# Kernel optimization log

Hardware: AMD Instinct MI355X
Metric: run time of the kernel (lower is better)

## Reference

```python
import jax, jax.numpy as jnp
import numpy as np

D_MODEL = 1024
N_HEADS = 16
D_HEAD = D_MODEL // N_HEADS
B, T = 4, 2048


def setup_inputs() -> dict:
    key = jax.random.key(0)
    ks = jax.random.split(key, 5)
    scale = 1.0 / np.sqrt(D_MODEL)
    return {
        "x": jax.random.normal(ks[0], (B, T, D_MODEL), dtype=jnp.float32),
        "W_Q": jax.random.normal(ks[1], (D_MODEL, D_MODEL), dtype=jnp.float32) * scale,
        "W_K": jax.random.normal(ks[2], (D_MODEL, D_MODEL), dtype=jnp.float32) * scale,
        "W_V": jax.random.normal(ks[3], (D_MODEL, D_MODEL), dtype=jnp.float32) * scale,
        "W_O": jax.random.normal(ks[4], (D_MODEL, D_MODEL), dtype=jnp.float32) * scale,
    }


def reference(x, W_Q, W_K, W_V, W_O):
    b, t, c = x.shape
    # nn.Linear applies x @ W.T; weights stored [out, in]
    def heads(w):
        return (x @ w.T).reshape(b, t, N_HEADS, D_HEAD).transpose(0, 2, 1, 3)  # b h t d
    q, k, v = heads(W_Q), heads(W_K), heads(W_V)
    scores = jnp.einsum("bhqd,bhkd->bhqk", q, k) / jnp.sqrt(jnp.float32(D_HEAD))
    causal = jnp.tril(jnp.ones((t, t), dtype=bool))
    scores = jnp.where(causal, scores, -jnp.inf)
    attn = jax.nn.softmax(scores, axis=-1)
    out = jnp.einsum("bhqk,bhkd->bhqd", attn, v)
    out = out.transpose(0, 2, 1, 3).reshape(b, t, c)
    return out @ W_O.T
```

## Files before the change

kernel.cpp:

```cpp
#include <hip/hip_runtime.h>
#include <stdint.h>
#include <stddef.h>

#define SEQ 2048
#define NH 16
#define DH 64
#define DM 1024
#define NROWS 8192

typedef __attribute__((ext_vector_type(4))) float f32x4;
typedef __attribute__((ext_vector_type(16))) float f32x16;
typedef __attribute__((ext_vector_type(8))) short s16x8;
typedef __attribute__((ext_vector_type(4))) unsigned u32x4;

__device__ __forceinline__ unsigned short f2bf(float f) {
  unsigned int u = __builtin_bit_cast(unsigned int, f);
  u += 0x7fffu + ((u >> 16) & 1u);
  return (unsigned short)(u >> 16);
}

__device__ __forceinline__ float exp2fast(float x) {
#if __has_builtin(__builtin_amdgcn_exp2f)
  return __builtin_amdgcn_exp2f(x);
#else
  return exp2f(x);
#endif
}

__device__ __forceinline__ float rcpfast(float x) {
#if __has_builtin(__builtin_amdgcn_rcpf)
  return __builtin_amdgcn_rcpf(x);
#else
  return 1.0f / x;
#endif
}

__device__ __forceinline__ unsigned pk2(float lo, float hi) {
  return __builtin_amdgcn_perm(__builtin_bit_cast(unsigned, hi),
                               __builtin_bit_cast(unsigned, lo), 0x07060302u);
}


__device__ __forceinline__ void async16(const void* g, void* l) {
  __builtin_amdgcn_global_load_lds(
      (const __attribute__((address_space(1))) unsigned int*)g,
      (__attribute__((address_space(3))) unsigned int*)l, 16, 0, 0);
}

__global__ __launch_bounds__(256) void cast_all(const float* __restrict__ x,
                                                const float* __restrict__ w0,
                                                const float* __restrict__ w1,
                                                const float* __restrict__ w2,
                                                const float* __restrict__ w3,
                                                short* __restrict__ Xb,
                                                short* __restrict__ Wb) {
  int g = blockIdx.x * 256 + threadIdx.x;
  const float* src;
  short* dst;
  int off;
  if (g < NROWS * DM / 8) {
    src = x; dst = Xb; off = g;
  } else {
    int r = g - NROWS * DM / 8;
    int w = r >> 17;
    off = r & 131071;
    src = (w == 0) ? w0 : (w == 1) ? w1 : (w == 2) ? w2 : w3;
    dst = Wb + ((size_t)w << 20);
  }
  const float4* s4 = (const float4*)src;
  float4 a = s4[2 * off], b = s4[2 * off + 1];
  s16x8 o;
  o[0] = (short)f2bf(a.x); o[1] = (short)f2bf(a.y);
  o[2] = (short)f2bf(a.z); o[3] = (short)f2bf(a.w);
  o[4] = (short)f2bf(b.x); o[5] = (short)f2bf(b.y);
  o[6] = (short)f2bf(b.z); o[7] = (short)f2bf(b.w);
  *(s16x8*)(dst + (size_t)8 * off) = o;
}

__global__ __launch_bounds__(512, 2) void gemm_qkv(const short* __restrict__ X,
                                                   const short* __restrict__ Wq,
                                                   const short* __restrict__ Wk,
                                                   const short* __restrict__ Wv,
                                                   short* __restrict__ Qo,
                                                   short* __restrict__ Ko,
                                                   short* __restrict__ Vo) {
  extern __shared__ __align__(16) short smem[];
  const int tid = threadIdx.x;
  const int lane = tid & 63, wave = tid >> 6;
  const int l15 = lane & 15, quad = lane >> 4;
  const int bn = blockIdx.x * 128;
  const int bm = blockIdx.y * 256;
  const int wm = (wave >> 1) * 64, wn = (wave & 1) * 64;

  const short* Ab = X + (size_t)bm * DM;
  const short* W0 = Wq + (size_t)bn * DM;
  const short* W1 = Wk + (size_t)bn * DM;
  const short* W2 = Wv + (size_t)bn * DM;

  f32x4 acc[3][4][4];
#pragma unroll
  for (int g = 0; g < 3; g++)
#pragma unroll
    for (int i = 0; i < 4; i++)
#pragma unroll
      for (int j = 0; j < 4; j++) acc[g][i][j] = (f32x4)0.f;

  auto stage = [&](int k, int buf) {
    short* base = smem + buf * 20480;
    const int k0 = k * 32;
#pragma unroll
    for (int i = 0; i < 2; i++) {
      int f = i * 512 + tid;
      int row = f >> 2;
      int c = ((f & 3) ^ (row & 3) ^ ((row >> 2) & 1)) * 8;
      async16(Ab + (size_t)row * DM + k0 + c, base + (size_t)f * 8);
    }
    {
      int f = tid;
      int row = f >> 2;
      int c = ((f & 3) ^ (row & 3) ^ ((row >> 2) & 1)) * 8;
      size_t go = (size_t)row * DM + k0 + c;
      async16(W0 + go, base + 8192 + (size_t)f * 8);
      async16(W1 + go, base + 12288 + (size_t)f * 8);
      async16(W2 + go, base + 16384 + (size_t)f * 8);
    }
  };

  stage(0, 0);
  __syncthreads();

  const int sl = (l15 & 3) ^ ((l15 >> 2) & 1);
  for (int k = 0; k < 32; k++) {
    const int buf = k & 1;
    if (k < 31) stage(k + 1, buf ^ 1);
    const short* base = smem + buf * 20480;

    s16x8 af[4];
#pragma unroll
    for (int t = 0; t < 4; t++)
      af[t] = *(const s16x8*)(base + (size_t)(wm + t * 16 + l15) * 32 + (size_t)((quad ^ sl) * 8));
#pragma unroll
    for (int g = 0; g < 3; g++) {
      const short* wb = base + 8192 + g * 4096;
      s16x8 bfr[4];
#pragma unroll
      for (int t = 0; t < 4; t++)
        bfr[t] = *(const s16x8*)(wb + (size_t)(wn + t * 16 + l15) * 32 + (size_t)((quad ^ sl) * 8));
#pragma unroll
      for (int mt = 0; mt < 4; mt++)
#pragma unroll
        for (int nt = 0; nt < 4; nt++) {
          if (g == 2)
            acc[2][mt][nt] = __builtin_amdgcn_mfma_f32_16x16x32_bf16(bfr[nt], af[mt], acc[2][mt][nt], 0, 0, 0);
          else
            acc[g][mt][nt] = __builtin_amdgcn_mfma_f32_16x16x32_bf16(af[mt], bfr[nt], acc[g][mt][nt], 0, 0, 0);
        }
    }
    __syncthreads();
  }

#pragma unroll
  for (int g = 0; g < 2; g++) {
    short* Dst = g ? Ko : Qo;
#pragma unroll
    for (int mt = 0; mt < 4; mt++)
#pragma unroll
      for (int r = 0; r < 4; r++)
#pragma unroll
        for (int nt = 0; nt < 4; nt++) {
          int m = bm + wm + mt * 16 + quad * 4 + r;
          int n = bn + wn + nt * 16 + l15;
          int b = m >> 11, t = m & (SEQ - 1);
          int hh = n >> 6, d = n & 63;
          Dst[((((size_t)b * NH + hh) * SEQ + t) << 6) + d] = (short)f2bf(acc[g][mt][nt][r]);
        }
  }
#pragma unroll
  for (int mt = 0; mt < 4; mt++)
#pragma unroll
    for (int r = 0; r < 4; r++)
#pragma unroll
      for (int nt = 0; nt < 4; nt++) {
        int n = bn + wn + nt * 16 + quad * 4 + r;
        int m = bm + wm + mt * 16 + l15;
        int b = m >> 11, t = m & (SEQ - 1);
        int hh = n >> 6, d = n & 63;
        Vo[(((size_t)b * NH + hh) * DH + d) * SEQ + t] = (short)f2bf(acc[2][mt][nt][r]);
      }
}

__global__ __launch_bounds__(256, 2) void gemm_o(const short* __restrict__ A,
                                                 const short* __restrict__ B,
                                                 float* __restrict__ C) {
  __shared__ __align__(16) short As[256 * 64];
  __shared__ __align__(16) short Bs[128 * 64];
  const int tid = threadIdx.x;
  const int lane = tid & 63, wave = tid >> 6;
  const int l15 = lane & 15, quad = lane >> 4;
  const int bm = blockIdx.y * 256, bn = blockIdx.x * 128;
  const int wm = (wave >> 1) * 128, wn = (wave & 1) * 64;

  const short* Ab = A + (size_t)bm * DM;
  const short* Bb = B + (size_t)bn * DM;

  f32x4 acc[8][4];
#pragma unroll
  for (int i = 0; i < 8; i++)
#pragma unroll
    for (int j = 0; j < 4; j++) acc[i][j] = (f32x4)0.f;

  for (int k0 = 0; k0 < DM; k0 += 64) {
#pragma unroll
    for (int i = 0; i < 8; i++) {
      int f = i * 256 + tid;
      int row = f >> 3, c = ((f & 7) ^ (row & 7)) * 8;
      async16(Ab + (size_t)row * DM + k0 + c, As + (size_t)f * 8);
    }
#pragma unroll
    for (int i = 0; i < 4; i++) {
      int f = i * 256 + tid;
      int row = f >> 3, c = ((f & 7) ^ (row & 7)) * 8;
      async16(Bb + (size_t)row * DM + k0 + c, Bs + (size_t)f * 8);
    }
    __syncthreads();
#pragma unroll
    for (int ks = 0; ks < 2; ks++) {
      s16x8 bfr[4];
#pragma unroll
      for (int t = 0; t < 4; t++)
        bfr[t] = *(const s16x8*)(Bs + (wn + t * 16 + l15) * 64 + (((ks * 4 + quad) ^ (l15 & 7)) * 8));
#pragma unroll
      for (int mt = 0; mt < 8; mt++) {
        s16x8 af = *(const s16x8*)(As + (wm + mt * 16 + l15) * 64 + (((ks * 4 + quad) ^ (l15 & 7)) * 8));
#pragma unroll
        for (int nt = 0; nt < 4; nt++)
          acc[mt][nt] = __builtin_amdgcn_mfma_f32_16x16x32_bf16(af, bfr[nt], acc[mt][nt], 0, 0, 0);
      }
    }
    __syncthreads();
  }

#pragma unroll
  for (int mt = 0; mt < 8; mt++)
#pragma unroll
    for (int r = 0; r < 4; r++) {
      int m = bm + wm + mt * 16 + quad * 4 + r;
#pragma unroll
      for (int nt = 0; nt < 4; nt++)
        C[(size_t)m * DM + bn + wn + nt * 16 + l15] = acc[mt][nt][r];
    }
}

__global__ __launch_bounds__(256, 2) void attn_kernel(const short* __restrict__ Q,
                                                      const short* __restrict__ K,
                                                      const short* __restrict__ V,
                                                      short* __restrict__ O) {
  __shared__ __align__(16) short Smem[2 * 16384];

  const int tid = threadIdx.x;
  const int lane = tid & 63, wave = tid >> 6;
  const int l31 = lane & 31, h = lane >> 5;

  const int r = blockIdx.x & 63;
  const int qt = 15 - (blockIdx.x >> 6);
  const int bh = (r & 7) * 8 + (r >> 3);
  const int q0 = qt * 128;

  const short* Qb = Q + (size_t)bh * SEQ * DH;
  const short* Kb = K + (size_t)bh * SEQ * DH;
  const short* Vb = V + (size_t)bh * DH * SEQ;

  auto stageK = [&](int ktile, int buf) {
    short* base = Smem + buf * 16384;
    const short* ksrc = Kb + (size_t)ktile * 128 * DH;
#pragma unroll
    for (int i = 0; i < 4; i++) {
      int f = i * 256 + tid;
      int kk = f >> 3, c8 = (f & 7) ^ (kk & 7);
      async16(ksrc + (size_t)kk * DH + c8 * 8, base + (size_t)f * 8);
    }
  };
  auto stageV = [&](int ktile, int buf) {
    short* base = Smem + buf * 16384 + 8192;
    const short* vsrc = Vb + (size_t)ktile * 128;
#pragma unroll
    for (int i = 0; i < 4; i++) {
      int f = i * 256 + tid;
      int d = f >> 4, c16 = (f & 15) ^ (d & 15);
      async16(vsrc + (size_t)d * SEQ + c16 * 8, base + (size_t)f * 8);
    }
  };

  s16x8 qf[4];
#pragma unroll
  for (int ks = 0; ks < 4; ks++)
    qf[ks] = *(const s16x8*)(Qb + (size_t)(q0 + wave * 32 + l31) * DH + ks * 16 + h * 8);

  f32x16 oacc[2];
  oacc[0] = (f32x16)0.f;
  oacc[1] = (f32x16)0.f;
  float m_own = -3.0e38f, l_own = 0.f, aprev = 0.f;
  s16x8 pf[8];
  const float C = 0.18033688011112042f;

  stageK(0, 0);

  for (int kt = 0; kt <= qt; kt++) {
    const int cur = kt & 1;
    __syncthreads();
    if (kt < qt) stageK(kt + 1, cur ^ 1);
    stageV(kt, cur);
    const short* Ks = Smem + cur * 16384;

    f32x16 sacc[4];
#pragma unroll
    for (int T = 0; T < 4; T++) sacc[T] = (f32x16)0.f;
#pragma unroll
    for (int ks = 0; ks < 4; ks++) {
#pragma unroll
      for (int T = 0; T < 4; T++) {
        s16x8 kf = *(const s16x8*)(Ks + (T * 32 + l31) * 64 + (((2 * ks + h) ^ (l31 & 7)) * 8));
        sacc[T] = __builtin_amdgcn_mfma_f32_32x32x16_bf16(kf, qf[ks], sacc[T], 0, 0, 0);
      }
    }

    if (kt > 0) {
      const short* Vp = Smem + (cur ^ 1) * 16384 + 8192;
#pragma unroll
      for (int r2 = 0; r2 < 16; r2++) {
        oacc[0][r2] *= aprev;
        oacc[1][r2] *= aprev;
      }
#pragma unroll
      for (int kc = 0; kc < 8; kc++) {
#pragma unroll
        for (int td = 0; td < 2; td++) {
          s16x8 vf = *(const s16x8*)(Vp + (td * 32 + l31) * 128 + (((2 * kc + h) ^ (l31 & 15)) * 8));
          oacc[td] = __builtin_amdgcn_mfma_f32_32x32x16_bf16(vf, pf[kc], oacc[td], 0, 0, 0);
        }
      }
    }

    if (kt == qt) {
      int limit = wave * 32 + l31 - 4 * h;
#pragma unroll
      for (int T = 0; T < 4; T++)
#pragma unroll
        for (int r2 = 0; r2 < 16; r2++) {
          int kkc = T * 32 + (r2 & 3) + 8 * (r2 >> 2);
          if (kkc > limit) sacc[T][r2] = -3.0e38f;
        }
    }

    float tm[4];
#pragma unroll
    for (int T = 0; T < 4; T++) {
      float a = fmaxf(fmaxf(sacc[T][0], sacc[T][1]), fmaxf(sacc[T][2], sacc[T][3]));
      float b = fmaxf(fmaxf(sacc[T][4], sacc[T][5]), fmaxf(sacc[T][6], sacc[T][7]));
      float cc = fmaxf(fmaxf(sacc[T][8], sacc[T][9]), fmaxf(sacc[T][10], sacc[T][11]));
      float d = fmaxf(fmaxf(sacc[T][12], sacc[T][13]), fmaxf(sacc[T][14], sacc[T][15]));
      tm[T] = fmaxf(fmaxf(a, b), fmaxf(cc, d));
    }
    float mx = fmaxf(fmaxf(tm[0], tm[1]), fmaxf(tm[2], tm[3]));
    mx = fmaxf(mx, __shfl_xor(mx, 32, 64));
    float mnew = fmaxf(m_own, mx);
    float mb = mnew * C;
    float alpha = exp2fast(m_own * C - mb);
    m_own = mnew;

    float ts[4];
#pragma unroll
    for (int T = 0; T < 4; T++) {
#pragma unroll
      for (int r2 = 0; r2 < 16; r2++) sacc[T][r2] = exp2fast(fmaf(sacc[T][r2], C, -mb));
      float a = (sacc[T][0] + sacc[T][1]) + (sacc[T][2] + sacc[T][3]);
      float b = (sacc[T][4] + sacc[T][5]) + (sacc[T][6] + sacc[T][7]);
      float cc = (sacc[T][8] + sacc[T][9]) + (sacc[T][10] + sacc[T][11]);
      float d = (sacc[T][12] + sacc[T][13]) + (sacc[T][14] + sacc[T][15]);
      ts[T] = (a + b) + (cc + d);
    }
    float rsum = (ts[0] + ts[1]) + (ts[2] + ts[3]);
    rsum += __shfl_xor(rsum, 32, 64);
    l_own = l_own * alpha + rsum;

#pragma unroll
    for (int T = 0; T < 4; T++) {
      unsigned P0 = pk2(sacc[T][0], sacc[T][1]);
      unsigned P1 = pk2(sacc[T][2], sacc[T][3]);
      unsigned P2 = pk2(sacc[T][4], sacc[T][5]);
      unsigned P3 = pk2(sacc[T][6], sacc[T][7]);
      unsigned P4 = pk2(sacc[T][8], sacc[T][9]);
      unsigned P5 = pk2(sacc[T][10], sacc[T][11]);
      unsigned P6 = pk2(sacc[T][12], sacc[T][13]);
      unsigned P7 = pk2(sacc[T][14], sacc[T][15]);
      unsigned R0 = (unsigned)__shfl_xor((int)(h ? P0 : P2), 32, 64);
      unsigned R1 = (unsigned)__shfl_xor((int)(h ? P1 : P3), 32, 64);
      unsigned R2 = (unsigned)__shfl_xor((int)(h ? P4 : P6), 32, 64);
      unsigned R3 = (unsigned)__shfl_xor((int)(h ? P5 : P7), 32, 64);
      u32x4 lo, hi;
      lo[0] = h ? R0 : P0; lo[1] = h ? R1 : P1; lo[2] = h ? P2 : R0; lo[3] = h ? P3 : R1;
      hi[0] = h ? R2 : P4; hi[1] = h ? R3 : P5; hi[2] = h ? P6 : R2; hi[3] = h ? P7 : R3;
      pf[2 * T] = __builtin_bit_cast(s16x8, lo);
      pf[2 * T + 1] = __builtin_bit_cast(s16x8, hi);
    }

    aprev = alpha;
  }

  __syncthreads();
  {
    const short* Vp = Smem + (qt & 1) * 16384 + 8192;
#pragma unroll
    for (int r2 = 0; r2 < 16; r2++) {
      oacc[0][r2] *= aprev;
      oacc[1][r2] *= aprev;
    }
#pragma unroll
    for (int kc = 0; kc < 8; kc++) {
#pragma unroll
      for (int td = 0; td < 2; td++) {
        s16x8 vf = *(const s16x8*)(Vp + (td * 32 + l31) * 128 + (((2 * kc + h) ^ (l31 & 15)) * 8));
        oacc[td] = __builtin_amdgcn_mfma_f32_32x32x16_bf16(vf, pf[kc], oacc[td], 0, 0, 0);
      }
    }
  }
  __syncthreads();

  const int b = bh >> 4, head = bh & 15;
  float inv = rcpfast(l_own);
  const int g = lane >> 3, d4 = (lane & 7) * 4;
#pragma unroll
  for (int td = 0; td < 2; td++) {
    float* tb = (float*)Smem + (size_t)(wave * 2 + td) * 1056;
#pragma unroll
    for (int r2 = 0; r2 < 16; r2++) {
      int d_loc = (r2 & 3) + 8 * (r2 >> 2) + 4 * h;
      tb[d_loc * 33 + l31] = oacc[td][r2] * inv;
    }
#pragma unroll
    for (int j = 0; j < 4; j++) {
      int qq = j * 8 + g;
      float x0 = tb[(d4 + 0) * 33 + qq];
      float x1 = tb[(d4 + 1) * 33 + qq];
      float x2 = tb[(d4 + 2) * 33 + qq];
      float x3 = tb[(d4 + 3) * 33 + qq];
      uint2 pkd;
      pkd.x = (unsigned)f2bf(x0) | ((unsigned)f2bf(x1) << 16);
      pkd.y = (unsigned)f2bf(x2) | ((unsigned)f2bf(x3) << 16);
      int q = q0 + wave * 32 + qq;
      *(uint2*)(O + ((size_t)(b * SEQ + q)) * DM + head * DH + td * 32 + d4) = pkd;
    }
  }
}

extern "C" void kernel_launch(void* const* d_in, const int* in_sizes, int n_in,
                              void* d_out, int out_size, void* d_ws, size_t ws_size,
                              hipStream_t stream) {
  const float* x  = (const float*)d_in[0];
  const float* wq = (const float*)d_in[1];
  const float* wk = (const float*)d_in[2];
  const float* wv = (const float*)d_in[3];
  const float* wo = (const float*)d_in[4];

  short* ws = (short*)d_ws;
  short* Xb  = ws;
  short* Wqb = Xb + (size_t)NROWS * DM;
  short* Wkb = Wqb + (size_t)DM * DM;
  short* Wvb = Wkb + (size_t)DM * DM;
  short* Wob = Wvb + (size_t)DM * DM;
  short* Qb  = Wob + (size_t)DM * DM;
  short* Kb  = Qb + (size_t)NROWS * DM;
  short* Vtb = Kb + (size_t)NROWS * DM;
  short* Ob  = Xb;

  static bool attr_done = false;
  if (!attr_done) {
    (void)hipFuncSetAttribute((const void*)gemm_qkv,
                              hipFuncAttributeMaxDynamicSharedMemorySize, 81920);
    attr_done = true;
  }

  int total_chunks = NROWS * DM / 8 + 4 * (DM * DM / 8);
  cast_all<<<total_chunks / 256, 256, 0, stream>>>(x, wq, wk, wv, wo, Xb, Wqb);

  gemm_qkv<<<dim3(8, 32), 512, 81920, stream>>>(Xb, Wqb, Wkb, Wvb, Qb, Kb, Vtb);

  attn_kernel<<<1024, 256, 0, stream>>>(Qb, Kb, Vtb, Ob);

  gemm_o<<<dim3(8, 32), 256, 0, stream>>>(Ob, Wob, (float*)d_out);
}
```

Measured before the change: 245.1 us.

## Double-buffer gemm_o with 512 threads and 32-wide K stages

Rewrites the output-projection GEMM to use 8 waves per block, each owning a 64x64 sub-tile. The K loop now runs in 32-element steps with double-buffered shared memory, so the next stage's async loads are issued while the current stage's MFMAs execute. This is meant to hide global-load latency that was previously exposed behind a barrier every step. It uses a new XOR swizzle for the 32-wide rows and halves the accumulator registers per thread, at the cost of more barriers per unit of work.

Result: faster. 237.0 us (-3.3%).

```diff
diff --git a/kernel.cpp b/kernel.cpp
--- a/kernel.cpp
+++ b/kernel.cpp
@@ -189,59 +189,69 @@
       }
 }
 
-__global__ __launch_bounds__(256, 2) void gemm_o(const short* __restrict__ A,
+__global__ __launch_bounds__(512, 2) void gemm_o(const short* __restrict__ A,
                                                  const short* __restrict__ B,
                                                  float* __restrict__ C) {
-  __shared__ __align__(16) short As[256 * 64];
-  __shared__ __align__(16) short Bs[128 * 64];
+  __shared__ __align__(16) short smem[2 * 12288];
   const int tid = threadIdx.x;
   const int lane = tid & 63, wave = tid >> 6;
   const int l15 = lane & 15, quad = lane >> 4;
   const int bm = blockIdx.y * 256, bn = blockIdx.x * 128;
-  const int wm = (wave >> 1) * 128, wn = (wave & 1) * 64;
+  const int wm = (wave >> 1) * 64, wn = (wave & 1) * 64;
 
   const short* Ab = A + (size_t)bm * DM;
   const short* Bb = B + (size_t)bn * DM;
 
-  f32x4 acc[8][4];
-#pragma unroll
-  for (int i = 0; i < 8; i++)
+  f32x4 acc[4][4];
+#pragma unroll
+  for (int i = 0; i < 4; i++)
 #pragma unroll
     for (int j = 0; j < 4; j++) acc[i][j] = (f32x4)0.f;
 
-  for (int k0 = 0; k0 < DM; k0 += 64) {
-#pragma unroll
-    for (int i = 0; i < 8; i++) {
-      int f = i * 256 + tid;
-      int row = f >> 3, c = ((f & 7) ^ (row & 7)) * 8;
-      async16(Ab + (size_t)row * DM + k0 + c, As + (size_t)f * 8);
-    }
-#pragma unroll
-    for (int i = 0; i < 4; i++) {
-      int f = i * 256 + tid;
-      int row = f >> 3, c = ((f & 7) ^ (row & 7)) * 8;
-      async16(Bb + (size_t)row * DM + k0 + c, Bs + (size_t)f * 8);
-    }
+  auto stage = [&](int k, int buf) {
+    short* base = smem + buf * 12288;
+    const int k0 = k * 32;
+#pragma unroll
+    for (int i = 0; i < 2; i++) {
+      int f = i * 512 + tid;
+      int row = f >> 2;
+      int c = ((f & 3) ^ (row & 3) ^ ((row >> 2) & 1)) * 8;
+      async16(Ab + (size_t)row * DM + k0 + c, base + (size_t)f * 8);
+    }
+    {
+      int f = tid;
+      int row = f >> 2;
+      int c = ((f & 3) ^ (row & 3) ^ ((row >> 2) & 1)) * 8;
+      async16(Bb + (size_t)row * DM + k0 + c, base + 8192 + (size_t)f * 8);
+    }
+  };
+
+  stage(0, 0);
+  __syncthreads();
+
+  const int sl = (l15 & 3) ^ ((l15 >> 2) & 1);
+  for (int k = 0; k < 32; k++) {
+    const int buf = k & 1;
+    if (k < 31) stage(k + 1, buf ^ 1);
+    const short* base = smem + buf * 12288;
+
+    s16x8 af[4], bfr[4];
+#pragma unroll
+    for (int t = 0; t < 4; t++)
+      af[t] = *(const s16x8*)(base + (size_t)(wm + t * 16 + l15) * 32 + (size_t)((quad ^ sl) * 8));
+#pragma unroll
+    for (int t = 0; t < 4; t++)
+      bfr[t] = *(const s16x8*)(base + 8192 + (size_t)(wn + t * 16 + l15) * 32 + (size_t)((quad ^ sl) * 8));
+#pragma unroll
+    for (int mt = 0; mt < 4; mt++)
+#pragma unroll
+      for (int nt = 0; nt < 4; nt++)
+        acc[mt][nt] = __builtin_amdgcn_mfma_f32_16x16x32_bf16(af[mt], bfr[nt], acc[mt][nt], 0, 0, 0);
     __syncthreads();
-#pragma unroll
-    for (int ks = 0; ks < 2; ks++) {
-      s16x8 bfr[4];
-#pragma unroll
-      for (int t = 0; t < 4; t++)
-        bfr[t] = *(const s16x8*)(Bs + (wn + t * 16 + l15) * 64 + (((ks * 4 + quad) ^ (l15 & 7)) * 8));
-#pragma unroll
-      for (int mt = 0; mt < 8; mt++) {
-        s16x8 af = *(const s16x8*)(As + (wm + mt * 16 + l15) * 64 + (((ks * 4 + quad) ^ (l15 & 7)) * 8));
-#pragma unroll
-        for (int nt = 0; nt < 4; nt++)
-          acc[mt][nt] = __builtin_amdgcn_mfma_f32_16x16x32_bf16(af, bfr[nt], acc[mt][nt], 0, 0, 0);
-      }
-    }
-    __syncthreads();
-  }
-
-#pragma unroll
-  for (int mt = 0; mt < 8; mt++)
+  }
+
+#pragma unroll
+  for (int mt = 0; mt < 4; mt++)
 #pragma unroll
     for (int r = 0; r < 4; r++) {
       int m = bm + wm + mt * 16 + quad * 4 + r;
@@ -487,5 +497,5 @@
 
   attn_kernel<<<1024, 256, 0, stream>>>(Qb, Kb, Vtb, Ob);
 
-  gemm_o<<<dim3(8, 32), 256, 0, stream>>>(Ob, Wob, (float*)d_out);
-}
+  gemm_o<<<dim3(8, 32), 512, 0, stream>>>(Ob, Wob, (float*)d_out);
+}
```
